# Optimization experiments

Hardware: AMD Instinct MI355X
Metric: run time of the kernel (lower is better)

The kernel has to match this reference:

```python
import jax, jax.numpy as jnp
import numpy as np

TEMPERATURE = 0.5


def _nt_xent(emb_i, emb_j, temperature):
    n = emb_i.shape[0]
    reps = jnp.concatenate([emb_i, emb_j], axis=0)  # [2N, D]
    # cosine similarity via normalized GEMM (same math as broadcasted F.cosine_similarity)
    eps = 1e-8
    norms = jnp.maximum(jnp.linalg.norm(reps, axis=1, keepdims=True), eps)
    z = reps / norms
    sim = z @ z.T  # [2N, 2N]
    # positives: sim[k, k+N] for k<N and sim[k, k-N] for k>=N
    sim_ij = jnp.diagonal(sim, offset=n)
    sim_ji = jnp.diagonal(sim, offset=-n)
    positives = jnp.concatenate([sim_ij, sim_ji], axis=0)  # [2N]
    logits = sim / temperature
    # mask out self-similarity (diagonal) in denominator
    neg_mask = 1.0 - jnp.eye(2 * n, dtype=logits.dtype)
    denom = jnp.sum(neg_mask * jnp.exp(logits), axis=1)  # [2N]
    loss_partial = -(positives / temperature - jnp.log(denom))
    return jnp.sum(loss_partial) / (2 * n)


def setup_inputs() -> dict:
    key = jax.random.key(0)
    k1, k2 = jax.random.split(key)
    N, D = 4096, 256
    emb_i = jax.random.normal(k1, (N, D), dtype=jnp.float32)
    emb_j = jax.random.normal(k2, (N, D), dtype=jnp.float32)
    return {"emb_i": emb_i, "emb_j": emb_j}


def reference(emb_i, emb_j):
    return _nt_xent(emb_i, emb_j, TEMPERATURE)
```

## Files before the change

kernel.cpp:

```cpp
#include <hip/hip_runtime.h>
#include <hip/hip_bf16.h>
#include <math.h>

#define D      256
#define N2     8192
#define NHALF  4096
#define TILE   128
#define BK     64
#define NCH    4
#define LDW    68
#define NTRI   2080
#define TPB    512

typedef __bf16 bf16x8_t __attribute__((ext_vector_type(8)));
typedef __bf16 bf16x4_t __attribute__((ext_vector_type(4)));
typedef float  f32x4_t  __attribute__((ext_vector_type(4)));

__global__ __launch_bounds__(256) void prep_kernel(const float* __restrict__ a,
                                                   const float* __restrict__ b,
                                                   __bf16* __restrict__ zb,
                                                   float* __restrict__ g_pos,
                                                   float* __restrict__ g_denom,
                                                   unsigned* __restrict__ g_t1) {
    const int tid = threadIdx.x;
    const int gt  = blockIdx.x * 256 + tid;
    if (gt < N2) g_denom[gt] = 0.0f;
    if (gt < 65 * 32 + 1) g_t1[gt] = 0u;

    const int w = blockIdx.x * 4 + (tid >> 6);
    const int l = tid & 63;
    float4 x = ((const float4*)(a + (size_t)w * D))[l];
    float4 y = ((const float4*)(b + (size_t)w * D))[l];
    float sxx = x.x * x.x + x.y * x.y + x.z * x.z + x.w * x.w;
    float syy = y.x * y.x + y.y * y.y + y.z * y.z + y.w * y.w;
    float sxy = x.x * y.x + x.y * y.y + x.z * y.z + x.w * y.w;
    #pragma unroll
    for (int off = 32; off; off >>= 1) {
        sxx += __shfl_xor(sxx, off, 64);
        syy += __shfl_xor(syy, off, 64);
        sxy += __shfl_xor(sxy, off, 64);
    }
    const float rx = 1.0f / fmaxf(sqrtf(sxx), 1e-8f);
    const float ry = 1.0f / fmaxf(sqrtf(syy), 1e-8f);

    bf16x4_t ox, oy;
    ox[0] = (__bf16)(x.x * rx); ox[1] = (__bf16)(x.y * rx);
    ox[2] = (__bf16)(x.z * rx); ox[3] = (__bf16)(x.w * rx);
    oy[0] = (__bf16)(y.x * ry); oy[1] = (__bf16)(y.y * ry);
    oy[2] = (__bf16)(y.z * ry); oy[3] = (__bf16)(y.w * ry);
    *(bf16x4_t*)(zb + (size_t)w * D + l * 4)           = ox;
    *(bf16x4_t*)(zb + (size_t)(w + NHALF) * D + l * 4) = oy;

    if (l == 0) {
        const float p = sxy * rx * ry;
        g_pos[w]         = p;
        g_pos[w + NHALF] = p;
    }
}

__global__ __launch_bounds__(TPB, 4) void sim_kernel(const __bf16* __restrict__ zb,
                                                     float* __restrict__ g_denom,
                                                     const float* __restrict__ g_pos,
                                                     unsigned* __restrict__ g_t1,
                                                     float* __restrict__ out) {
    __shared__ __bf16 ldsA[2][TILE * LDW];
    __shared__ __bf16 ldsB[2][TILE * LDW];
    __shared__ float  sw[8];
    __shared__ bool   amLast;

    const int tid    = threadIdx.x;
    const int l      = tid & 63;
    const int lane15 = l & 15;
    const int quad   = l >> 4;
    const int w      = tid >> 6;
    const int wr     = (w & 3) * 32;
    const int wc     = (w >> 2) * 64;

    const int k = blockIdx.x;
    int bi = (int)(64.5f - sqrtf(64.5f * 64.5f - 2.0f * (float)k));
    while ((bi * (129 - bi)) / 2 > k) --bi;
    while (((bi + 1) * (128 - bi)) / 2 <= k) ++bi;
    const int bj   = bi + (k - (bi * (129 - bi)) / 2);
    const bool diag = (bi == bj);

    const int r = tid >> 2;
    const int q = tid & 3;
    const __bf16* ga = zb + (size_t)(bi * TILE + r) * D + q * 16;
    const __bf16* gb = zb + (size_t)(bj * TILE + r) * D + q * 16;
    const int wofs = r * LDW + q * 16;

    bf16x8_t sa0, sa1, sb0, sb1;
    auto load_regs = [&](int c) {
        const int k0 = c * BK;
        sa0 = *(const bf16x8_t*)(ga + k0);
        sa1 = *(const bf16x8_t*)(ga + k0 + 8);
        sb0 = *(const bf16x8_t*)(gb + k0);
        sb1 = *(const bf16x8_t*)(gb + k0 + 8);
    };
    auto write_lds = [&](int buf) {
        *(bf16x8_t*)(&ldsA[buf][wofs])     = sa0;
        *(bf16x8_t*)(&ldsA[buf][wofs + 8]) = sa1;
        *(bf16x8_t*)(&ldsB[buf][wofs])     = sb0;
        *(bf16x8_t*)(&ldsB[buf][wofs + 8]) = sb1;
    };

    f32x4_t acc[2][4];
    #pragma unroll
    for (int mi = 0; mi < 2; ++mi)
        #pragma unroll
        for (int nj = 0; nj < 4; ++nj)
            acc[mi][nj] = (f32x4_t){0.f, 0.f, 0.f, 0.f};

    auto compute = [&](int buf) {
        #pragma unroll
        for (int ks = 0; ks < 2; ++ks) {
            bf16x8_t af[2], bff[4];
            #pragma unroll
            for (int mi = 0; mi < 2; ++mi)
                af[mi] = *(const bf16x8_t*)(&ldsA[buf][(wr + mi * 16 + lane15) * LDW + ks * 32 + quad * 8]);
            #pragma unroll
            for (int nj = 0; nj < 4; ++nj)
                bff[nj] = *(const bf16x8_t*)(&ldsB[buf][(wc + nj * 16 + lane15) * LDW + ks * 32 + quad * 8]);
            #pragma unroll
            for (int mi = 0; mi < 2; ++mi)
                #pragma unroll
                for (int nj = 0; nj < 4; ++nj)
                    acc[mi][nj] = __builtin_amdgcn_mfma_f32_16x16x32_bf16(bff[nj], af[mi], acc[mi][nj], 0, 0, 0);
        }
    };

    load_regs(0);
    write_lds(0);
    __syncthreads();

    int cur = 0;
    #pragma unroll
    for (int c = 0; c < NCH; ++c) {
        if (c + 1 < NCH) load_regs(c + 1);
        compute(cur);
        if (c + 1 < NCH) {
            write_lds(cur ^ 1);
            __syncthreads();
            cur ^= 1;
        }
    }

    float rs[2] = {0.f, 0.f};
    float cp[4][4];
    #pragma unroll
    for (int nj = 0; nj < 4; ++nj)
        #pragma unroll
        for (int t = 0; t < 4; ++t) cp[nj][t] = 0.f;

    #pragma unroll
    for (int mi = 0; mi < 2; ++mi) {
        #pragma unroll
        for (int nj = 0; nj < 4; ++nj) {
            const bool dn = diag && (wr + mi * 16 == wc + nj * 16);
            #pragma unroll
            for (int t = 0; t < 4; ++t) {
                float e = exp2f(acc[mi][nj][t] * 2.8853900817779268f);
                if (dn && (quad * 4 + t) == lane15) e = 0.0f;
                rs[mi] += e;
                cp[nj][t] += e;
            }
        }
    }
    #pragma unroll
    for (int mi = 0; mi < 2; ++mi) {
        rs[mi] += __shfl_xor(rs[mi], 16, 64);
        rs[mi] += __shfl_xor(rs[mi], 32, 64);
    }
    if (l < 16) {
        #pragma unroll
        for (int mi = 0; mi < 2; ++mi)
            atomicAdd(&g_denom[bi * TILE + wr + mi * 16 + l], rs[mi]);
    }
    if (!diag) {
        float s8[8], s4[4], s2[2], s;
        #pragma unroll
        for (int i = 0; i < 8; ++i) {
            const float lo = cp[i >> 2][i & 3];
            const float hi = cp[(i + 8) >> 2][(i + 8) & 3];
            const float send = (lane15 & 8) ? lo : hi;
            const float recv = __shfl_xor(send, 8, 64);
            s8[i] = ((lane15 & 8) ? hi : lo) + recv;
        }
        #pragma unroll
        for (int i = 0; i < 4; ++i) {
            const float send = (lane15 & 4) ? s8[i] : s8[i + 4];
            const float recv = __shfl_xor(send, 4, 64);
            s4[i] = ((lane15 & 4) ? s8[i + 4] : s8[i]) + recv;
        }
        #pragma unroll
        for (int i = 0; i < 2; ++i) {
            const float send = (lane15 & 2) ? s4[i] : s4[i + 2];
            const float recv = __shfl_xor(send, 2, 64);
            s2[i] = ((lane15 & 2) ? s4[i + 2] : s4[i]) + recv;
        }
        {
            const float send = (lane15 & 1) ? s2[0] : s2[1];
            const float recv = __shfl_xor(send, 1, 64);
            s = ((lane15 & 1) ? s2[1] : s2[0]) + recv;
        }
        atomicAdd(&g_denom[bj * TILE + wc + (lane15 >> 2) * 16 + quad * 4 + (lane15 & 3)], s);
    }

    __syncthreads();
    if (tid == 0) {
        asm volatile("s_waitcnt vmcnt(0)" ::: "memory");
        unsigned t1 = __hip_atomic_fetch_add(&g_t1[(blockIdx.x >> 5) * 32], 1u,
                                             __ATOMIC_RELAXED, __HIP_MEMORY_SCOPE_AGENT);
        bool grpLast = (t1 == 31);
        unsigned t2 = 0;
        if (grpLast)
            t2 = __hip_atomic_fetch_add(&g_t1[65 * 32], 1u, __ATOMIC_RELAXED,
                                        __HIP_MEMORY_SCOPE_AGENT);
        amLast = grpLast && (t2 == 64);
    }
    __syncthreads();
    if (!amLast) return;

    float local = 0.0f;
    for (int kk = tid; kk < N2; kk += TPB) {
        float dn = __hip_atomic_load(&g_denom[kk], __ATOMIC_RELAXED,
                                     __HIP_MEMORY_SCOPE_AGENT);
        local += logf(dn) - 2.0f * g_pos[kk];
    }
    #pragma unroll
    for (int off = 32; off; off >>= 1) local += __shfl_xor(local, off, 64);
    if (l == 0) sw[w] = local;
    __syncthreads();
    if (tid == 0) {
        float s = 0.f;
        #pragma unroll
        for (int i = 0; i < 8; ++i) s += sw[i];
        out[0] = s / (float)N2;
    }
}

extern "C" void kernel_launch(void* const* d_in, const int* in_sizes, int n_in,
                              void* d_out, int out_size, void* d_ws, size_t ws_size,
                              hipStream_t stream) {
    const float* emb_i = (const float*)d_in[0];
    const float* emb_j = (const float*)d_in[1];

    __bf16*   zb      = (__bf16*)d_ws;
    float*    g_denom = (float*)((char*)d_ws + (size_t)N2 * D * 2);
    float*    g_pos   = g_denom + N2;
    unsigned* g_t1    = (unsigned*)(g_pos + N2);
    float*    out     = (float*)d_out;

    prep_kernel<<<NHALF / 4, 256, 0, stream>>>(emb_i, emb_j, zb, g_pos, g_denom, g_t1);
    sim_kernel<<<NTRI, TPB, 0, stream>>>(zb, g_denom, g_pos, g_t1, out);
}
```

Before: 100.8 us.

## Load A fragments directly from global into registers and remap block order

The A-tile operands are now loaded from global memory straight into MFMA register fragments, double-buffered across K chunks. This removes the A tile from LDS, halving shared-memory traffic and the LDS footprint, which may raise occupancy. Block indices are also permuted so that blocks running at the same time, which are likely spread across XCDs, take strided triangle tiles, which may improve L2 locality and load balance. The cost is uncoalesced 16-byte global loads for A and higher register pressure.

```diff
diff --git a/kernel.cpp b/kernel.cpp
--- a/kernel.cpp
+++ b/kernel.cpp
@@ -63,7 +63,6 @@
                                                      const float* __restrict__ g_pos,
                                                      unsigned* __restrict__ g_t1,
                                                      float* __restrict__ out) {
-    __shared__ __bf16 ldsA[2][TILE * LDW];
     __shared__ __bf16 ldsB[2][TILE * LDW];
     __shared__ float  sw[8];
     __shared__ bool   amLast;
@@ -76,7 +75,8 @@
     const int wr     = (w & 3) * 32;
     const int wc     = (w >> 2) * 64;
 
-    const int k = blockIdx.x;
+    const int bx = blockIdx.x;
+    const int k  = (bx & 7) * 260 + (bx >> 3);
     int bi = (int)(64.5f - sqrtf(64.5f * 64.5f - 2.0f * (float)k));
     while ((bi * (129 - bi)) / 2 > k) --bi;
     while (((bi + 1) * (128 - bi)) / 2 <= k) ++bi;
@@ -85,25 +85,29 @@
 
     const int r = tid >> 2;
     const int q = tid & 3;
-    const __bf16* ga = zb + (size_t)(bi * TILE + r) * D + q * 16;
     const __bf16* gb = zb + (size_t)(bj * TILE + r) * D + q * 16;
     const int wofs = r * LDW + q * 16;
 
-    bf16x8_t sa0, sa1, sb0, sb1;
-    auto load_regs = [&](int c) {
+    bf16x8_t sb0, sb1;
+    auto loadB = [&](int c) {
         const int k0 = c * BK;
-        sa0 = *(const bf16x8_t*)(ga + k0);
-        sa1 = *(const bf16x8_t*)(ga + k0 + 8);
         sb0 = *(const bf16x8_t*)(gb + k0);
         sb1 = *(const bf16x8_t*)(gb + k0 + 8);
     };
-    auto write_lds = [&](int buf) {
-        *(bf16x8_t*)(&ldsA[buf][wofs])     = sa0;
-        *(bf16x8_t*)(&ldsA[buf][wofs + 8]) = sa1;
+    auto writeB = [&](int buf) {
         *(bf16x8_t*)(&ldsB[buf][wofs])     = sb0;
         *(bf16x8_t*)(&ldsB[buf][wofs + 8]) = sb1;
     };
 
+    const __bf16* abase = zb + (size_t)(bi * TILE + wr + lane15) * D + quad * 8;
+    auto loadA = [&](int c, bf16x8_t (&af)[2][2]) {
+        #pragma unroll
+        for (int mi = 0; mi < 2; ++mi)
+            #pragma unroll
+            for (int ks = 0; ks < 2; ++ks)
+                af[mi][ks] = *(const bf16x8_t*)(abase + (size_t)mi * 16 * D + c * BK + ks * 32);
+    };
+
     f32x4_t acc[2][4];
     #pragma unroll
     for (int mi = 0; mi < 2; ++mi)
@@ -111,13 +115,10 @@
         for (int nj = 0; nj < 4; ++nj)
             acc[mi][nj] = (f32x4_t){0.f, 0.f, 0.f, 0.f};
 
-    auto compute = [&](int buf) {
+    auto compute = [&](int buf, const bf16x8_t (&af)[2][2]) {
         #pragma unroll
         for (int ks = 0; ks < 2; ++ks) {
-            bf16x8_t af[2], bff[4];
-            #pragma unroll
-            for (int mi = 0; mi < 2; ++mi)
-                af[mi] = *(const bf16x8_t*)(&ldsA[buf][(wr + mi * 16 + lane15) * LDW + ks * 32 + quad * 8]);
+            bf16x8_t bff[4];
             #pragma unroll
             for (int nj = 0; nj < 4; ++nj)
                 bff[nj] = *(const bf16x8_t*)(&ldsB[buf][(wc + nj * 16 + lane15) * LDW + ks * 32 + quad * 8]);
@@ -125,25 +126,29 @@
             for (int mi = 0; mi < 2; ++mi)
                 #pragma unroll
                 for (int nj = 0; nj < 4; ++nj)
-                    acc[mi][nj] = __builtin_amdgcn_mfma_f32_16x16x32_bf16(bff[nj], af[mi], acc[mi][nj], 0, 0, 0);
-        }
-    };
-
-    load_regs(0);
-    write_lds(0);
-    __syncthreads();
-
-    int cur = 0;
-    #pragma unroll
-    for (int c = 0; c < NCH; ++c) {
-        if (c + 1 < NCH) load_regs(c + 1);
-        compute(cur);
+                    acc[mi][nj] = __builtin_amdgcn_mfma_f32_16x16x32_bf16(bff[nj], af[mi][ks], acc[mi][nj], 0, 0, 0);
+        }
+    };
+
+    bf16x8_t afA[2][2], afB[2][2];
+
+    loadA(0, afA);
+    loadB(0);
+    writeB(0);
+    __syncthreads();
+
+    auto step = [&](int c, const bf16x8_t (&afC)[2][2], bf16x8_t (&afN)[2][2], int buf) {
+        if (c + 1 < NCH) { loadB(c + 1); loadA(c + 1, afN); }
+        compute(buf, afC);
         if (c + 1 < NCH) {
-            write_lds(cur ^ 1);
+            writeB(buf ^ 1);
             __syncthreads();
-            cur ^= 1;
-        }
-    }
+        }
+    };
+    step(0, afA, afB, 0);
+    step(1, afB, afA, 1);
+    step(2, afA, afB, 0);
+    step(3, afB, afA, 1);
 
     float rs[2] = {0.f, 0.f};
     float cp[4][4];
@@ -209,7 +214,7 @@
     __syncthreads();
     if (tid == 0) {
         asm volatile("s_waitcnt vmcnt(0)" ::: "memory");
-        unsigned t1 = __hip_atomic_fetch_add(&g_t1[(blockIdx.x >> 5) * 32], 1u,
+        unsigned t1 = __hip_atomic_fetch_add(&g_t1[(bx >> 5) * 32], 1u,
                                              __ATOMIC_RELAXED, __HIP_MEMORY_SCOPE_AGENT);
         bool grpLast = (t1 == 31);
         unsigned t2 = 0;
```

After: 112.4 us. 11.5% more time.

## Use 4 waves with 64x64 per-wave tiles and XCD-aware block remapping

Applied to the files above, without the earlier changes.

The sim kernel drops from 512 to 256 threads per block, and each wave now computes a 64x64 sub-tile (4x4 MFMA fragments) instead of 32x64. This raises register-level reuse of the LDS fragments, so fewer LDS reads are needed per MFMA. The block index is also remapped so that consecutive tiles land on the same XCD, which is meant to improve L2 locality of the shared row panels. The cost is more accumulator registers per thread and fewer waves to hide latency, under launch bounds of (256, 2).

```diff
diff --git a/kernel.cpp b/kernel.cpp
--- a/kernel.cpp
+++ b/kernel.cpp
@@ -10,7 +10,6 @@
 #define NCH    4
 #define LDW    68
 #define NTRI   2080
-#define TPB    512
 
 typedef __bf16 bf16x8_t __attribute__((ext_vector_type(8)));
 typedef __bf16 bf16x4_t __attribute__((ext_vector_type(4)));
@@ -58,14 +57,14 @@
     }
 }
 
-__global__ __launch_bounds__(TPB, 4) void sim_kernel(const __bf16* __restrict__ zb,
+__global__ __launch_bounds__(256, 2) void sim_kernel(const __bf16* __restrict__ zb,
                                                      float* __restrict__ g_denom,
                                                      const float* __restrict__ g_pos,
                                                      unsigned* __restrict__ g_t1,
                                                      float* __restrict__ out) {
     __shared__ __bf16 ldsA[2][TILE * LDW];
     __shared__ __bf16 ldsB[2][TILE * LDW];
-    __shared__ float  sw[8];
+    __shared__ float  sw[4];
     __shared__ bool   amLast;
 
     const int tid    = threadIdx.x;
@@ -73,40 +72,43 @@
     const int lane15 = l & 15;
     const int quad   = l >> 4;
     const int w      = tid >> 6;
-    const int wr     = (w & 3) * 32;
-    const int wc     = (w >> 2) * 64;
-
-    const int k = blockIdx.x;
+    const int wr     = (w >> 1) * 64;
+    const int wc     = (w & 1) * 64;
+
+    const int bx = blockIdx.x;
+    const int k  = (bx & 7) * 260 + (bx >> 3);
     int bi = (int)(64.5f - sqrtf(64.5f * 64.5f - 2.0f * (float)k));
     while ((bi * (129 - bi)) / 2 > k) --bi;
     while (((bi + 1) * (128 - bi)) / 2 <= k) ++bi;
     const int bj   = bi + (k - (bi * (129 - bi)) / 2);
     const bool diag = (bi == bj);
 
-    const int r = tid >> 2;
-    const int q = tid & 3;
-    const __bf16* ga = zb + (size_t)(bi * TILE + r) * D + q * 16;
-    const __bf16* gb = zb + (size_t)(bj * TILE + r) * D + q * 16;
-    const int wofs = r * LDW + q * 16;
-
-    bf16x8_t sa0, sa1, sb0, sb1;
+    const int r    = tid >> 1;
+    const int half = tid & 1;
+    const __bf16* ga = zb + (size_t)(bi * TILE + r) * D + half * 32;
+    const __bf16* gb = zb + (size_t)(bj * TILE + r) * D + half * 32;
+    const int wofs = r * LDW + half * 32;
+
+    bf16x8_t sa[4], sb[4];
     auto load_regs = [&](int c) {
         const int k0 = c * BK;
-        sa0 = *(const bf16x8_t*)(ga + k0);
-        sa1 = *(const bf16x8_t*)(ga + k0 + 8);
-        sb0 = *(const bf16x8_t*)(gb + k0);
-        sb1 = *(const bf16x8_t*)(gb + k0 + 8);
+        #pragma unroll
+        for (int u = 0; u < 4; ++u) {
+            sa[u] = *(const bf16x8_t*)(ga + k0 + u * 8);
+            sb[u] = *(const bf16x8_t*)(gb + k0 + u * 8);
+        }
     };
     auto write_lds = [&](int buf) {
-        *(bf16x8_t*)(&ldsA[buf][wofs])     = sa0;
-        *(bf16x8_t*)(&ldsA[buf][wofs + 8]) = sa1;
-        *(bf16x8_t*)(&ldsB[buf][wofs])     = sb0;
-        *(bf16x8_t*)(&ldsB[buf][wofs + 8]) = sb1;
+        #pragma unroll
+        for (int u = 0; u < 4; ++u) {
+            *(bf16x8_t*)(&ldsA[buf][wofs + u * 8]) = sa[u];
+            *(bf16x8_t*)(&ldsB[buf][wofs + u * 8]) = sb[u];
+        }
     };
 
-    f32x4_t acc[2][4];
-    #pragma unroll
-    for (int mi = 0; mi < 2; ++mi)
+    f32x4_t acc[4][4];
+    #pragma unroll
+    for (int mi = 0; mi < 4; ++mi)
         #pragma unroll
         for (int nj = 0; nj < 4; ++nj)
             acc[mi][nj] = (f32x4_t){0.f, 0.f, 0.f, 0.f};
@@ -114,15 +116,15 @@
     auto compute = [&](int buf) {
         #pragma unroll
         for (int ks = 0; ks < 2; ++ks) {
-            bf16x8_t af[2], bff[4];
-            #pragma unroll
-            for (int mi = 0; mi < 2; ++mi)
+            bf16x8_t af[4], bff[4];
+            #pragma unroll
+            for (int mi = 0; mi < 4; ++mi)
                 af[mi] = *(const bf16x8_t*)(&ldsA[buf][(wr + mi * 16 + lane15) * LDW + ks * 32 + quad * 8]);
             #pragma unroll
             for (int nj = 0; nj < 4; ++nj)
                 bff[nj] = *(const bf16x8_t*)(&ldsB[buf][(wc + nj * 16 + lane15) * LDW + ks * 32 + quad * 8]);
             #pragma unroll
-            for (int mi = 0; mi < 2; ++mi)
+            for (int mi = 0; mi < 4; ++mi)
                 #pragma unroll
                 for (int nj = 0; nj < 4; ++nj)
                     acc[mi][nj] = __builtin_amdgcn_mfma_f32_16x16x32_bf16(bff[nj], af[mi], acc[mi][nj], 0, 0, 0);
@@ -145,7 +147,7 @@
         }
     }
 
-    float rs[2] = {0.f, 0.f};
+    float rs[4] = {0.f, 0.f, 0.f, 0.f};
     float cp[4][4];
     #pragma unroll
     for (int nj = 0; nj < 4; ++nj)
@@ -153,7 +155,7 @@
         for (int t = 0; t < 4; ++t) cp[nj][t] = 0.f;
 
     #pragma unroll
-    for (int mi = 0; mi < 2; ++mi) {
+    for (int mi = 0; mi < 4; ++mi) {
         #pragma unroll
         for (int nj = 0; nj < 4; ++nj) {
             const bool dn = diag && (wr + mi * 16 == wc + nj * 16);
@@ -167,13 +169,13 @@
         }
     }
     #pragma unroll
-    for (int mi = 0; mi < 2; ++mi) {
+    for (int mi = 0; mi < 4; ++mi) {
         rs[mi] += __shfl_xor(rs[mi], 16, 64);
         rs[mi] += __shfl_xor(rs[mi], 32, 64);
     }
     if (l < 16) {
         #pragma unroll
-        for (int mi = 0; mi < 2; ++mi)
+        for (int mi = 0; mi < 4; ++mi)
             atomicAdd(&g_denom[bi * TILE + wr + mi * 16 + l], rs[mi]);
     }
     if (!diag) {
@@ -209,7 +211,7 @@
     __syncthreads();
     if (tid == 0) {
         asm volatile("s_waitcnt vmcnt(0)" ::: "memory");
-        unsigned t1 = __hip_atomic_fetch_add(&g_t1[(blockIdx.x >> 5) * 32], 1u,
+        unsigned t1 = __hip_atomic_fetch_add(&g_t1[(bx >> 5) * 32], 1u,
                                              __ATOMIC_RELAXED, __HIP_MEMORY_SCOPE_AGENT);
         bool grpLast = (t1 == 31);
         unsigned t2 = 0;
@@ -222,7 +224,7 @@
     if (!amLast) return;
 
     float local = 0.0f;
-    for (int kk = tid; kk < N2; kk += TPB) {
+    for (int kk = tid; kk < N2; kk += 256) {
         float dn = __hip_atomic_load(&g_denom[kk], __ATOMIC_RELAXED,
                                      __HIP_MEMORY_SCOPE_AGENT);
         local += logf(dn) - 2.0f * g_pos[kk];
@@ -231,12 +233,7 @@
     for (int off = 32; off; off >>= 1) local += __shfl_xor(local, off, 64);
     if (l == 0) sw[w] = local;
     __syncthreads();
-    if (tid == 0) {
-        float s = 0.f;
-        #pragma unroll
-        for (int i = 0; i < 8; ++i) s += sw[i];
-        out[0] = s / (float)N2;
-    }
+    if (tid == 0) out[0] = (sw[0] + sw[1] + sw[2] + sw[3]) / (float)N2;
 }
 
 extern "C" void kernel_launch(void* const* d_in, const int* in_sizes, int n_in,
@@ -252,5 +249,5 @@
     float*    out     = (float*)d_out;
 
     prep_kernel<<<NHALF / 4, 256, 0, stream>>>(emb_i, emb_j, zb, g_pos, g_denom, g_t1);
-    sim_kernel<<<NTRI, TPB, 0, stream>>>(zb, g_denom, g_pos, g_t1, out);
+    sim_kernel<<<NTRI, 256, 0, stream>>>(zb, g_denom, g_pos, g_t1, out);
 }
```

Measured after the change: 107.1 us. 6.3% more time.

## Fuse normalization prep into sim kernel with per-panel claim flags

Applied to the files above, without the earlier changes.

Removes the separate prep kernel. Each sim block normalizes the row panels it needs on demand: blocks race with compare-and-swap on per-panel flags, the winner writes bf16 rows, and losers spin until the panel is ready or fall back to doing it themselves. Positives are now read from the GEMM accumulators of the blocks where bj equals bi plus 32, and the scratch counters are zeroed with a memset. This saves a kernel launch and one pass over the inputs, but adds spin-waiting, a memset launch, and relies on relaxed atomic stores being visible across blocks.

```diff
diff --git a/kernel.cpp b/kernel.cpp
--- a/kernel.cpp
+++ b/kernel.cpp
@@ -13,59 +13,20 @@
 #define TPB    512
 
 typedef __bf16 bf16x8_t __attribute__((ext_vector_type(8)));
-typedef __bf16 bf16x4_t __attribute__((ext_vector_type(4)));
 typedef float  f32x4_t  __attribute__((ext_vector_type(4)));
 
-__global__ __launch_bounds__(256) void prep_kernel(const float* __restrict__ a,
-                                                   const float* __restrict__ b,
-                                                   __bf16* __restrict__ zb,
-                                                   float* __restrict__ g_pos,
-                                                   float* __restrict__ g_denom,
-                                                   unsigned* __restrict__ g_t1) {
-    const int tid = threadIdx.x;
-    const int gt  = blockIdx.x * 256 + tid;
-    if (gt < N2) g_denom[gt] = 0.0f;
-    if (gt < 65 * 32 + 1) g_t1[gt] = 0u;
-
-    const int w = blockIdx.x * 4 + (tid >> 6);
-    const int l = tid & 63;
-    float4 x = ((const float4*)(a + (size_t)w * D))[l];
-    float4 y = ((const float4*)(b + (size_t)w * D))[l];
-    float sxx = x.x * x.x + x.y * x.y + x.z * x.z + x.w * x.w;
-    float syy = y.x * y.x + y.y * y.y + y.z * y.z + y.w * y.w;
-    float sxy = x.x * y.x + x.y * y.y + x.z * y.z + x.w * y.w;
-    #pragma unroll
-    for (int off = 32; off; off >>= 1) {
-        sxx += __shfl_xor(sxx, off, 64);
-        syy += __shfl_xor(syy, off, 64);
-        sxy += __shfl_xor(sxy, off, 64);
-    }
-    const float rx = 1.0f / fmaxf(sqrtf(sxx), 1e-8f);
-    const float ry = 1.0f / fmaxf(sqrtf(syy), 1e-8f);
-
-    bf16x4_t ox, oy;
-    ox[0] = (__bf16)(x.x * rx); ox[1] = (__bf16)(x.y * rx);
-    ox[2] = (__bf16)(x.z * rx); ox[3] = (__bf16)(x.w * rx);
-    oy[0] = (__bf16)(y.x * ry); oy[1] = (__bf16)(y.y * ry);
-    oy[2] = (__bf16)(y.z * ry); oy[3] = (__bf16)(y.w * ry);
-    *(bf16x4_t*)(zb + (size_t)w * D + l * 4)           = ox;
-    *(bf16x4_t*)(zb + (size_t)(w + NHALF) * D + l * 4) = oy;
-
-    if (l == 0) {
-        const float p = sxy * rx * ry;
-        g_pos[w]         = p;
-        g_pos[w + NHALF] = p;
-    }
-}
-
-__global__ __launch_bounds__(TPB, 4) void sim_kernel(const __bf16* __restrict__ zb,
+__global__ __launch_bounds__(TPB, 4) void sim_kernel(const float* __restrict__ a,
+                                                     const float* __restrict__ b,
+                                                     __bf16* __restrict__ zb,
                                                      float* __restrict__ g_denom,
-                                                     const float* __restrict__ g_pos,
+                                                     float* __restrict__ g_pos,
                                                      unsigned* __restrict__ g_t1,
+                                                     unsigned* __restrict__ g_flag,
                                                      float* __restrict__ out) {
     __shared__ __bf16 ldsA[2][TILE * LDW];
     __shared__ __bf16 ldsB[2][TILE * LDW];
     __shared__ float  sw[8];
+    __shared__ int    clm;
     __shared__ bool   amLast;
 
     const int tid    = threadIdx.x;
@@ -76,12 +37,82 @@
     const int wr     = (w & 3) * 32;
     const int wc     = (w >> 2) * 64;
 
-    const int k = blockIdx.x;
+    const int bx = blockIdx.x;
+    const int k  = bx;
     int bi = (int)(64.5f - sqrtf(64.5f * 64.5f - 2.0f * (float)k));
     while ((bi * (129 - bi)) / 2 > k) --bi;
     while (((bi + 1) * (128 - bi)) / 2 <= k) ++bi;
     const int bj   = bi + (k - (bi * (129 - bi)) / 2);
     const bool diag = (bi == bj);
+
+    auto prep_panel = [&](int panel) {
+        const int pr = tid >> 2;
+        const int pq = tid & 3;
+        const int g  = panel * TILE + pr;
+        const float* src = (g < NHALF) ? (a + (size_t)g * D + pq * 64)
+                                       : (b + (size_t)(g - NHALF) * D + pq * 64);
+        float ss = 0.f;
+        #pragma unroll
+        for (int i = 0; i < 16; ++i) {
+            f32x4_t v = *(const f32x4_t*)(src + i * 4);
+            ss += v[0]*v[0] + v[1]*v[1] + v[2]*v[2] + v[3]*v[3];
+        }
+        ss += __shfl_xor(ss, 1, 64);
+        ss += __shfl_xor(ss, 2, 64);
+        const float rn = 1.0f / fmaxf(sqrtf(ss), 1e-8f);
+        unsigned* dst = (unsigned*)(zb + (size_t)g * D) + pq * 32;
+        #pragma unroll
+        for (int i = 0; i < 16; ++i) {
+            f32x4_t v = *(const f32x4_t*)(src + i * 4);
+            #pragma unroll
+            for (int e = 0; e < 2; ++e) {
+                __bf16 lo = (__bf16)(v[2*e]     * rn);
+                __bf16 hi = (__bf16)(v[2*e + 1] * rn);
+                unsigned u = ((unsigned)(*(unsigned short*)&hi) << 16)
+                           | (unsigned)(*(unsigned short*)&lo);
+                __hip_atomic_store(dst + i * 2 + e, u, __ATOMIC_RELAXED,
+                                   __HIP_MEMORY_SCOPE_AGENT);
+            }
+        }
+    };
+    auto claim = [&](int panel) {
+        if (tid == 0) {
+            unsigned exp0 = 0u;
+            bool won = __hip_atomic_compare_exchange_strong(
+                &g_flag[panel], &exp0, 1u, __ATOMIC_RELAXED, __ATOMIC_RELAXED,
+                __HIP_MEMORY_SCOPE_AGENT);
+            clm = won ? 0 : (int)exp0;
+        }
+        __syncthreads();
+        const int st = clm;
+        if (st == 0) {
+            prep_panel(panel);
+            __syncthreads();
+            if (tid == 0)
+                __hip_atomic_store(&g_flag[panel], 2u, __ATOMIC_RELAXED,
+                                   __HIP_MEMORY_SCOPE_AGENT);
+        } else if (st == 1) {
+            if (tid == 0) {
+                int it = 0;
+                while (__hip_atomic_load(&g_flag[panel], __ATOMIC_RELAXED,
+                                         __HIP_MEMORY_SCOPE_AGENT) != 2u
+                       && it < 300000) {
+                    __builtin_amdgcn_s_sleep(4);
+                    ++it;
+                }
+                clm = (__hip_atomic_load(&g_flag[panel], __ATOMIC_RELAXED,
+                                         __HIP_MEMORY_SCOPE_AGENT) == 2u) ? 2 : 3;
+            }
+            __syncthreads();
+            if (clm == 3) {
+                prep_panel(panel);
+                __syncthreads();
+            }
+        }
+        __syncthreads();
+    };
+    claim(bi);
+    if (!diag) claim(bj);
 
     const int r = tid >> 2;
     const int q = tid & 3;
@@ -145,6 +176,7 @@
         }
     }
 
+    const bool posBlk = (bj == bi + 32);
     float rs[2] = {0.f, 0.f};
     float cp[4][4];
     #pragma unroll
@@ -156,11 +188,17 @@
     for (int mi = 0; mi < 2; ++mi) {
         #pragma unroll
         for (int nj = 0; nj < 4; ++nj) {
-            const bool dn = diag && (wr + mi * 16 == wc + nj * 16);
+            const bool fd = (wr + mi * 16 == wc + nj * 16);
+            const bool dn = diag && fd;
+            const bool dp = posBlk && fd;
             #pragma unroll
             for (int t = 0; t < 4; ++t) {
                 float e = exp2f(acc[mi][nj][t] * 2.8853900817779268f);
                 if (dn && (quad * 4 + t) == lane15) e = 0.0f;
+                if (dp && (quad * 4 + t) == lane15)
+                    __hip_atomic_store(&g_pos[bi * TILE + wr + mi * 16 + lane15],
+                                       acc[mi][nj][t], __ATOMIC_RELAXED,
+                                       __HIP_MEMORY_SCOPE_AGENT);
                 rs[mi] += e;
                 cp[nj][t] += e;
             }
@@ -209,7 +247,7 @@
     __syncthreads();
     if (tid == 0) {
         asm volatile("s_waitcnt vmcnt(0)" ::: "memory");
-        unsigned t1 = __hip_atomic_fetch_add(&g_t1[(blockIdx.x >> 5) * 32], 1u,
+        unsigned t1 = __hip_atomic_fetch_add(&g_t1[(bx >> 5) * 32], 1u,
                                              __ATOMIC_RELAXED, __HIP_MEMORY_SCOPE_AGENT);
         bool grpLast = (t1 == 31);
         unsigned t2 = 0;
@@ -225,7 +263,12 @@
     for (int kk = tid; kk < N2; kk += TPB) {
         float dn = __hip_atomic_load(&g_denom[kk], __ATOMIC_RELAXED,
                                      __HIP_MEMORY_SCOPE_AGENT);
-        local += logf(dn) - 2.0f * g_pos[kk];
+        local += logf(dn);
+        if (kk < NHALF) {
+            float p = __hip_atomic_load(&g_pos[kk], __ATOMIC_RELAXED,
+                                        __HIP_MEMORY_SCOPE_AGENT);
+            local -= 4.0f * p;
+        }
     }
     #pragma unroll
     for (int off = 32; off; off >>= 1) local += __shfl_xor(local, off, 64);
@@ -245,12 +288,14 @@
     const float* emb_i = (const float*)d_in[0];
     const float* emb_j = (const float*)d_in[1];
 
-    __bf16*   zb      = (__bf16*)d_ws;
-    float*    g_denom = (float*)((char*)d_ws + (size_t)N2 * D * 2);
-    float*    g_pos   = g_denom + N2;
-    unsigned* g_t1    = (unsigned*)(g_pos + N2);
+    float*    g_denom = (float*)d_ws;
+    unsigned* g_t1    = (unsigned*)(g_denom + N2);
+    unsigned* g_flag  = g_t1 + 2088;
+    __bf16*   zb      = (__bf16*)((char*)d_ws + 41472);
+    float*    g_pos   = (float*)(zb + (size_t)N2 * D);
     float*    out     = (float*)d_out;
 
-    prep_kernel<<<NHALF / 4, 256, 0, stream>>>(emb_i, emb_j, zb, g_pos, g_denom, g_t1);
-    sim_kernel<<<NTRI, TPB, 0, stream>>>(zb, g_denom, g_pos, g_t1, out);
+    hipMemsetAsync(d_ws, 0, (size_t)(N2 * 4 + 2088 * 4 + 64 * 4), stream);
+    sim_kernel<<<NTRI, TPB, 0, stream>>>(emb_i, emb_j, zb, g_denom, g_pos,
+                                         g_t1, g_flag, out);
 }
```

Result: slower. 204.6 us (+102.9%).
